# Kernel tuning notes

Measured on AMD Instinct MI355X. Metric: run time of the kernel, lower is better.

## Reference

```python
import jax, jax.numpy as jnp
import numpy as np

SEQ, BATCH, IN, RES = 1024, 64, 512, 2048

def setup_inputs() -> dict:
    key = jax.random.key(0)
    k1, k2, k3, k4 = jax.random.split(key, 4)
    x = jax.random.normal(k1, (SEQ, BATCH, IN), dtype=jnp.float32)
    # ESN reservoir weights: untrained random matrices (spectral-radius style scaling)
    W_in = jax.random.normal(k2, (RES, IN), dtype=jnp.float32) * 0.1
    W_hh = jax.random.normal(k3, (RES, RES), dtype=jnp.float32) * (0.9 / jnp.sqrt(RES))
    b = jax.random.normal(k4, (RES,), dtype=jnp.float32) * 0.1
    return {"x": x, "W_in": W_in, "W_hh": W_hh, "b": b}

def reference(x, W_in, W_hh, b):
    # ESNBase.forward -> _forward_type_2 with num_layers=1, unidirectional.
    # h_t = tanh(x_t @ W_in^T + h_{t-1} @ W_hh^T + b)
    batch = x.shape[1]
    h0 = jnp.zeros((batch, W_hh.shape[0]), dtype=x.dtype)
    # Precompute input projection for all steps (parallel GEMM), scan the recurrence.
    xin = jnp.einsum('sbi,ri->sbr', x, W_in) + b  # (seq, batch, res)
    def step(h, u):
        h_new = jnp.tanh(u + h @ W_hh.T)
        return h_new, h_new
    h_n, states = jax.lax.scan(step, h0, xin)
    # output: (seq, batch, num_directions*hidden); h_n: (num_layers*num_directions, batch, hidden)
    return states, h_n[None, :, :]
```

## Files before the change

### kernel.cpp

```cpp
#include <hip/hip_runtime.h>
#include <hip/hip_bf16.h>


#define SEQ 1024
#define NB  64
#define INF 512
#define RES 2048

typedef float    f32x4 __attribute__((ext_vector_type(4)));
typedef _Float16 f16x8 __attribute__((ext_vector_type(8)));

__global__ __launch_bounds__(256) void xin_gemm(
    const float* __restrict__ X, const float* __restrict__ Win,
    const float* __restrict__ bias, float* __restrict__ U)
{
  __shared__ _Float16 lA[2][128][40];
  __shared__ _Float16 lB[2][128][40];

  const int tid  = threadIdx.x;
  const int lane = tid & 63;
  const int wv   = tid >> 6;
  const int wr   = wv >> 1;
  const int wc   = wv & 1;
  const int m0   = (blockIdx.x >> 4) * 128;
  const int n0   = (blockIdx.x & 15) * 128;

  const int srow = tid >> 1;
  const int sk   = (tid & 1) * 16;

  const int fr = lane & 15;
  const int fk = (lane >> 4) * 8;

  f32x4 acc[4][4] = {};
  float ra[16], rb[16];

  const float* xa_base = X   + (size_t)(m0 + srow) * INF + sk;
  const float* xb_base = Win + (size_t)(n0 + srow) * INF + sk;

#define LOADK(kt) do {                                                     \
    const float* pa = xa_base + (kt) * 32;                                 \
    const float* pb = xb_base + (kt) * 32;                                 \
    *(f32x4*)&ra[0]  = *(const f32x4*)(pa + 0);                            \
    *(f32x4*)&ra[4]  = *(const f32x4*)(pa + 4);                            \
    *(f32x4*)&ra[8]  = *(const f32x4*)(pa + 8);                            \
    *(f32x4*)&ra[12] = *(const f32x4*)(pa + 12);                           \
    *(f32x4*)&rb[0]  = *(const f32x4*)(pb + 0);                            \
    *(f32x4*)&rb[4]  = *(const f32x4*)(pb + 4);                            \
    *(f32x4*)&rb[8]  = *(const f32x4*)(pb + 8);                            \
    *(f32x4*)&rb[12] = *(const f32x4*)(pb + 12);                           \
  } while (0)

#define STOREK(buf) do {                                                   \
    f16x8 h0, h1;                                                          \
    _Pragma("unroll") for (int j = 0; j < 8; ++j) h0[j] = (_Float16)ra[j]; \
    _Pragma("unroll") for (int j = 0; j < 8; ++j) h1[j] = (_Float16)ra[8+j];\
    *(f16x8*)&lA[buf][srow][sk]     = h0;                                  \
    *(f16x8*)&lA[buf][srow][sk + 8] = h1;                                  \
    _Pragma("unroll") for (int j = 0; j < 8; ++j) h0[j] = (_Float16)rb[j]; \
    _Pragma("unroll") for (int j = 0; j < 8; ++j) h1[j] = (_Float16)rb[8+j];\
    *(f16x8*)&lB[buf][srow][sk]     = h0;                                  \
    *(f16x8*)&lB[buf][srow][sk + 8] = h1;                                  \
  } while (0)

#define COMPUTE(buf) do {                                                  \
    f16x8 af[4], bf[4];                                                    \
    _Pragma("unroll") for (int mt = 0; mt < 4; ++mt)                       \
      af[mt] = *(const f16x8*)&lA[buf][wr*64 + mt*16 + fr][fk];            \
    _Pragma("unroll") for (int nt = 0; nt < 4; ++nt)                       \
      bf[nt] = *(const f16x8*)&lB[buf][wc*64 + nt*16 + fr][fk];            \
    _Pragma("unroll") for (int mt = 0; mt < 4; ++mt)                       \
      _Pragma("unroll") for (int nt = 0; nt < 4; ++nt)                     \
        acc[mt][nt] = __builtin_amdgcn_mfma_f32_16x16x32_f16(              \
            af[mt], bf[nt], acc[mt][nt], 0, 0, 0);                         \
  } while (0)

  LOADK(0);
  STOREK(0);
  __syncthreads();

#pragma unroll 1
  for (int kt = 0; kt < 16; ++kt) {
    const int buf = kt & 1;
    if (kt < 15) LOADK(kt + 1);
    COMPUTE(buf);
    if (kt < 15) STOREK(buf ^ 1);
    __syncthreads();
  }

#pragma unroll
  for (int mt = 0; mt < 4; ++mt) {
    const int row = m0 + wr*64 + mt*16 + (lane >> 4) * 4;
#pragma unroll
    for (int nt = 0; nt < 4; ++nt) {
      const int col = n0 + wc*64 + nt*16 + fr;
      const float bv = bias[col];
#pragma unroll
      for (int i = 0; i < 4; ++i)
        U[(size_t)(row + i) * RES + col] = acc[mt][nt][i] + bv;
    }
  }
#undef LOADK
#undef STOREK
#undef COMPUTE
}

#define WPAD 2056

__global__ __launch_bounds__(512, 1) void esn_recur(
    const float* __restrict__ Whh, float* __restrict__ states,
    float* __restrict__ hn, _Float16* __restrict__ hbuf,
    unsigned* __restrict__ flags)
{
  __shared__ _Float16 Wl[32 * WPAD];
  __shared__ f32x4    red[2][7][64];

  const int tid  = threadIdx.x;
  const int lane = tid & 63;
  const int q    = tid >> 6;

  const int bid = blockIdx.x;
  const int xg  = bid & 7;
  const int bg  = xg >> 1;
  const int cg  = ((xg & 1) << 5) | (bid >> 3);
  const int b0  = bg * 16;
  const int c0  = cg * 32;

  {
    const int row = tid >> 4;
    const int ch  = tid & 15;
    const float* src = Whh + (size_t)(c0 + row) * RES + ch * 128;
    _Float16* dst = Wl + row * WPAD + ch * 128;
#pragma unroll 4
    for (int i = 0; i < 128; i += 4) {
      f32x4 v = *(const f32x4*)(src + i);
      dst[i + 0] = (_Float16)v.x;
      dst[i + 1] = (_Float16)v.y;
      dst[i + 2] = (_Float16)v.z;
      dst[i + 3] = (_Float16)v.w;
    }
  }
  __syncthreads();

  const int fr = lane & 15;
  const int fk = (lane >> 4) * 8;

  const _Float16* const wp0 = Wl + fr * WPAD + q * 256 + fk;
  const _Float16* const wp1 = wp0 + 16 * WPAD;

  _Float16* const hbuf0 = hbuf;
  _Float16* const hbuf1 = hbuf + (size_t)NB * RES;
  unsigned* const cnt = flags + bg * 64;

  for (int s = 0; s < SEQ; ++s) {
    f32x4 a0 = {0.f, 0.f, 0.f, 0.f}, a1 = {0.f, 0.f, 0.f, 0.f};

    float u[8];
    if (q == 0) {
      const float* up = states + (size_t)s * NB * RES;
#pragma unroll
      for (int t = 0; t < 8; ++t) {
        const int ct = t >> 2, i = t & 3;
        const int b  = b0 + (lane >> 4) * 4 + i;
        u[t] = up[(size_t)b * RES + c0 + ct * 16 + fr];
      }
    }

    if (s > 0) {
      const _Float16* hp = ((s & 1) ? hbuf0 : hbuf1)
                         + (size_t)(b0 + fr) * RES + q * 256 + fk;
#pragma unroll
      for (int ks = 0; ks < 8; ++ks) {
        union { unsigned long long w[2]; f16x8 v; } au;
        au.w[0] = __hip_atomic_load((const unsigned long long*)(hp + ks * 32),
                                    __ATOMIC_RELAXED, __HIP_MEMORY_SCOPE_AGENT);
        au.w[1] = __hip_atomic_load((const unsigned long long*)(hp + ks * 32 + 4),
                                    __ATOMIC_RELAXED, __HIP_MEMORY_SCOPE_AGENT);
        const f16x8 w0 = *(const f16x8*)(wp0 + ks * 32);
        const f16x8 w1 = *(const f16x8*)(wp1 + ks * 32);
        a0 = __builtin_amdgcn_mfma_f32_16x16x32_f16(au.v, w0, a0, 0, 0, 0);
        a1 = __builtin_amdgcn_mfma_f32_16x16x32_f16(au.v, w1, a1, 0, 0, 0);
      }
    }

    if (q > 0) { red[0][q - 1][lane] = a0; red[1][q - 1][lane] = a1; }
    __syncthreads();

    if (q == 0) {
#pragma unroll
      for (int j = 0; j < 7; ++j) { a0 += red[0][j][lane]; a1 += red[1][j][lane]; }

      float* up = states + (size_t)s * NB * RES;
      _Float16* hc = (s & 1) ? hbuf1 : hbuf0;
      unsigned short* hc16 = (unsigned short*)hc;
#pragma unroll
      for (int t = 0; t < 8; ++t) {
        const int ct = t >> 2, i = t & 3;
        const int b   = b0 + (lane >> 4) * 4 + i;
        const int col = c0 + ct * 16 + fr;
        const size_t off = (size_t)b * RES + col;
        const float v = tanhf(u[t] + (t < 4 ? a0[i] : a1[i]));
        up[off] = v;
        const _Float16 vh = (_Float16)v;
        __hip_atomic_store(&hc16[off], __builtin_bit_cast(unsigned short, vh),
                           __ATOMIC_RELAXED, __HIP_MEMORY_SCOPE_AGENT);
        if (s == SEQ - 1) hn[off] = v;
      }
      asm volatile("s_waitcnt vmcnt(0)" ::: "memory");
      if (lane == 0) {
        __hip_atomic_fetch_add(cnt, 1u, __ATOMIC_RELAXED, __HIP_MEMORY_SCOPE_AGENT);
        const unsigned target = 64u * (unsigned)(s + 1);
        while (__hip_atomic_load(cnt, __ATOMIC_RELAXED, __HIP_MEMORY_SCOPE_AGENT) < target)
          __builtin_amdgcn_s_sleep(2);
      }
    }
    __syncthreads();
  }
}

extern "C" void kernel_launch(void* const* d_in, const int* in_sizes, int n_in,
                              void* d_out, int out_size, void* d_ws, size_t ws_size,
                              hipStream_t stream) {
  const float* x    = (const float*)d_in[0];
  const float* W_in = (const float*)d_in[1];
  const float* W_hh = (const float*)d_in[2];
  const float* bias = (const float*)d_in[3];

  float* states = (float*)d_out;
  float* hn     = states + (size_t)SEQ * NB * RES;

  _Float16* hbuf  = (_Float16*)d_ws;
  unsigned* flags = (unsigned*)((char*)d_ws + (size_t)2 * NB * RES * sizeof(_Float16));

  hipMemsetAsync(flags, 0, 256 * sizeof(unsigned), stream);

  xin_gemm<<<dim3(512 * 16), dim3(256), 0, stream>>>(x, W_in, bias, states);
  esn_recur<<<dim3(256), dim3(512), 0, stream>>>(W_hh, states, hn, hbuf, flags);
}
```

Baseline: 7.565 ms.

## Replace atomic-counter barrier with per-wave flag polling and split epilogue across two waves

```diff
diff --git a/kernel.cpp b/kernel.cpp
--- a/kernel.cpp
+++ b/kernel.cpp
@@ -9,6 +9,11 @@
 
 typedef float    f32x4 __attribute__((ext_vector_type(4)));
 typedef _Float16 f16x8 __attribute__((ext_vector_type(8)));
+
+__device__ __forceinline__ float fast_tanh(float x) {
+  const float e = __expf(2.0f * x);
+  return 1.0f - 2.0f * __builtin_amdgcn_rcpf(1.0f + e);
+}
 
 __global__ __launch_bounds__(256) void xin_gemm(
     const float* __restrict__ X, const float* __restrict__ Win,
@@ -112,11 +117,13 @@
     unsigned* __restrict__ flags)
 {
   __shared__ _Float16 Wl[32 * WPAD];
-  __shared__ f32x4    red[2][7][64];
+  __shared__ f32x4    red0[8][64];
+  __shared__ f32x4    red1[8][64];
 
   const int tid  = threadIdx.x;
   const int lane = tid & 63;
-  const int q    = tid >> 6;
+  const int wv   = tid >> 6;
+  const int q    = wv;
 
   const int bid = blockIdx.x;
   const int xg  = bid & 7;
@@ -149,19 +156,19 @@
 
   _Float16* const hbuf0 = hbuf;
   _Float16* const hbuf1 = hbuf + (size_t)NB * RES;
-  unsigned* const cnt = flags + bg * 64;
+  unsigned* const fb = flags + bg * (128 * 32);
 
   for (int s = 0; s < SEQ; ++s) {
     f32x4 a0 = {0.f, 0.f, 0.f, 0.f}, a1 = {0.f, 0.f, 0.f, 0.f};
 
-    float u[8];
-    if (q == 0) {
+    float u[4];
+    if (wv < 2) {
       const float* up = states + (size_t)s * NB * RES;
-#pragma unroll
-      for (int t = 0; t < 8; ++t) {
-        const int ct = t >> 2, i = t & 3;
-        const int b  = b0 + (lane >> 4) * 4 + i;
-        u[t] = up[(size_t)b * RES + c0 + ct * 16 + fr];
+      const int col = c0 + wv * 16 + fr;
+#pragma unroll
+      for (int i = 0; i < 4; ++i) {
+        const int b = b0 + (lane >> 4) * 4 + i;
+        u[i] = up[(size_t)b * RES + col];
       }
     }
 
@@ -182,23 +189,24 @@
       }
     }
 
-    if (q > 0) { red[0][q - 1][lane] = a0; red[1][q - 1][lane] = a1; }
+    red0[q][lane] = a0;
+    red1[q][lane] = a1;
     __syncthreads();
 
-    if (q == 0) {
-#pragma unroll
-      for (int j = 0; j < 7; ++j) { a0 += red[0][j][lane]; a1 += red[1][j][lane]; }
+    if (wv < 2) {
+      const f32x4 (* __restrict__ rp)[64] = wv ? red1 : red0;
+      f32x4 acc = rp[0][lane];
+#pragma unroll
+      for (int j = 1; j < 8; ++j) acc += rp[j][lane];
 
       float* up = states + (size_t)s * NB * RES;
-      _Float16* hc = (s & 1) ? hbuf1 : hbuf0;
-      unsigned short* hc16 = (unsigned short*)hc;
-#pragma unroll
-      for (int t = 0; t < 8; ++t) {
-        const int ct = t >> 2, i = t & 3;
-        const int b   = b0 + (lane >> 4) * 4 + i;
-        const int col = c0 + ct * 16 + fr;
+      unsigned short* hc16 = (unsigned short*)((s & 1) ? hbuf1 : hbuf0);
+      const int col = c0 + wv * 16 + fr;
+#pragma unroll
+      for (int i = 0; i < 4; ++i) {
+        const int b = b0 + (lane >> 4) * 4 + i;
         const size_t off = (size_t)b * RES + col;
-        const float v = tanhf(u[t] + (t < 4 ? a0[i] : a1[i]));
+        const float v = fast_tanh(u[i] + acc[i]);
         up[off] = v;
         const _Float16 vh = (_Float16)v;
         __hip_atomic_store(&hc16[off], __builtin_bit_cast(unsigned short, vh),
@@ -206,11 +214,17 @@
         if (s == SEQ - 1) hn[off] = v;
       }
       asm volatile("s_waitcnt vmcnt(0)" ::: "memory");
-      if (lane == 0) {
-        __hip_atomic_fetch_add(cnt, 1u, __ATOMIC_RELAXED, __HIP_MEMORY_SCOPE_AGENT);
-        const unsigned target = 64u * (unsigned)(s + 1);
-        while (__hip_atomic_load(cnt, __ATOMIC_RELAXED, __HIP_MEMORY_SCOPE_AGENT) < target)
-          __builtin_amdgcn_s_sleep(2);
+      if (lane == 0)
+        __hip_atomic_store(fb + (wv * 64 + cg) * 32, (unsigned)(s + 1),
+                           __ATOMIC_RELAXED, __HIP_MEMORY_SCOPE_AGENT);
+    } else if (wv == 2) {
+      const unsigned tgt = (unsigned)(s + 1);
+      for (;;) {
+        const unsigned va = __hip_atomic_load(fb + lane * 32,
+                              __ATOMIC_RELAXED, __HIP_MEMORY_SCOPE_AGENT);
+        const unsigned vb = __hip_atomic_load(fb + (64 + lane) * 32,
+                              __ATOMIC_RELAXED, __HIP_MEMORY_SCOPE_AGENT);
+        if (__all((va >= tgt) & (vb >= tgt))) break;
       }
     }
     __syncthreads();
@@ -231,7 +245,7 @@
   _Float16* hbuf  = (_Float16*)d_ws;
   unsigned* flags = (unsigned*)((char*)d_ws + (size_t)2 * NB * RES * sizeof(_Float16));
 
-  hipMemsetAsync(flags, 0, 256 * sizeof(unsigned), stream);
+  hipMemsetAsync(flags, 0, (size_t)4 * 128 * 32 * sizeof(unsigned), stream);
 
   xin_gemm<<<dim3(512 * 16), dim3(256), 0, stream>>>(x, W_in, bias, states);
   esn_recur<<<dim3(256), dim3(512), 0, stream>>>(W_hh, states, hn, hbuf, flags);
```

Result: faster. 7.109 ms (-6.0%).
